# Kernel optimization log

Hardware: AMD Instinct MI355X
Metric: run time of the kernel (lower is better)

The kernel has to match this reference:

```python
import jax, jax.numpy as jnp
import numpy as np
from jax import lax

TS = 8          # texture cube resolution (hardcoded texture_size=8)
CHUNK = 336     # 13776 = 336 * 41, faces processed in scan chunks
EPS = 1e-8
INF = 1e30


def _project(vertices, K, R, t):
    # camera_mode='projection': v_cam = v @ R^T + t, then pinhole via K
    v_cam = vertices @ R.T + t            # [N,3]
    z = v_cam[:, 2]                        # [N]
    uvw = v_cam @ K.T                      # [N,3]
    xy = uvw[:, :2] / z[:, None]           # [N,2] pixel coords
    return xy, z


def _rasterize(xy, z, faces, H, W):
    # hard z-buffer rasterization, scanning over face chunks
    P = H * W
    px = jnp.arange(W, dtype=jnp.float32) + 0.5
    py = jnp.arange(H, dtype=jnp.float32) + 0.5
    pix_x = jnp.broadcast_to(px[None, :], (H, W)).reshape(P)
    pix_y = jnp.broadcast_to(py[:, None], (H, W)).reshape(P)

    nF = faces.shape[0]
    nchunks = nF // CHUNK
    fch = faces.reshape(nchunks, CHUNK, 3)
    offs = (jnp.arange(nchunks) * CHUNK).astype(jnp.int32)

    def step(carry, inp):
        zbuf, fid, wbuf = carry
        fc, off = inp
        tri = xy[fc]                       # [C,3,2]
        tz = z[fc]                         # [C,3]
        x0, y0 = tri[:, 0, 0][:, None], tri[:, 0, 1][:, None]
        x1, y1 = tri[:, 1, 0][:, None], tri[:, 1, 1][:, None]
        x2, y2 = tri[:, 2, 0][:, None], tri[:, 2, 1][:, None]
        denom = (y1 - y2) * (x0 - x2) + (x2 - x1) * (y0 - y2)   # [C,1]
        dsafe = jnp.where(jnp.abs(denom) > EPS, denom, 1.0)
        w0 = ((y1 - y2) * (pix_x - x2) + (x2 - x1) * (pix_y - y2)) / dsafe  # [C,P]
        w1 = ((y2 - y0) * (pix_x - x2) + (x0 - x2) * (pix_y - y2)) / dsafe
        w2 = 1.0 - w0 - w1
        valid = (jnp.abs(denom) > EPS) & (tz.min(axis=1, keepdims=True) > EPS)
        inside = (w0 >= 0) & (w1 >= 0) & (w2 >= 0) & valid
        # perspective-correct depth: 1/z = sum_i w_i / z_i
        inv_z = w0 / tz[:, 0:1] + w1 / tz[:, 1:2] + w2 / tz[:, 2:3]
        depth = jnp.where(inside & (inv_z > EPS), 1.0 / jnp.maximum(inv_z, EPS), INF)
        best = jnp.argmin(depth, axis=0)                         # [P]
        dmin = jnp.take_along_axis(depth, best[None, :], 0)[0]
        w0g = jnp.take_along_axis(w0, best[None, :], 0)[0]
        w1g = jnp.take_along_axis(w1, best[None, :], 0)[0]
        w2g = 1.0 - w0g - w1g
        wz = tz[best]                                            # [P,3]
        wc = jnp.stack([w0g, w1g, w2g], -1) / jnp.maximum(wz, EPS)
        wc = wc / jnp.maximum(wc.sum(-1, keepdims=True), EPS)    # persp-correct bary
        upd = dmin < zbuf
        zbuf = jnp.where(upd, dmin, zbuf)
        fid = jnp.where(upd, off + best.astype(jnp.int32), fid)
        wbuf = jnp.where(upd[:, None], wc, wbuf)
        return (zbuf, fid, wbuf), None

    init = (jnp.full((P,), INF, jnp.float32),
            jnp.full((P,), -1, jnp.int32),
            jnp.zeros((P, 3), jnp.float32))
    (zbuf, fid, wbuf), _ = lax.scan(step, init, (fch, offs))
    return fid, wbuf


def _sample_texture(texture, fid, bary):
    # trilinear sample of per-face texture cube [F,TS,TS,TS,3] at barycentric coords
    valid = fid >= 0
    f = jnp.where(valid, fid, 0)
    pos = jnp.clip(bary, 0.0, 1.0) * (TS - 1)
    i0 = jnp.clip(jnp.floor(pos), 0, TS - 2).astype(jnp.int32)   # [P,3]
    fr = pos - i0.astype(jnp.float32)
    flat = texture.reshape(-1, 3)
    base = f * (TS * TS * TS)
    out = jnp.zeros((fid.shape[0], 3), texture.dtype)
    for d0 in (0, 1):
        for d1 in (0, 1):
            for d2 in (0, 1):
                idx = base + (i0[:, 0] + d0) * TS * TS + (i0[:, 1] + d1) * TS + (i0[:, 2] + d2)
                w = ((fr[:, 0] if d0 else 1.0 - fr[:, 0])
                     * (fr[:, 1] if d1 else 1.0 - fr[:, 1])
                     * (fr[:, 2] if d2 else 1.0 - fr[:, 2]))
                out = out + w[:, None] * flat[idx]
    return out, valid


def setup_inputs() -> dict:
    key = jax.random.key(0)
    ks = jax.random.split(key, 4)
    n_verts, n_faces = 6890, 13776
    rs = 256
    vertices = 0.3 * jax.random.normal(ks[0], (n_verts, 3), jnp.float32)
    focal, c = 280.0, rs / 2.0
    K = jnp.array([[focal, 0.0, c], [0.0, focal, c], [0.0, 0.0, 1.0]], jnp.float32)
    R = jnp.eye(3, dtype=jnp.float32)
    t = jnp.array([0.0, 0.0, 2.5], jnp.float32)
    bgcolor = 255.0 * jax.random.uniform(ks[1], (3,), jnp.float32)
    texture = jax.random.normal(ks[2], (n_faces, TS, TS, TS, 3), jnp.float32)
    faces = jax.random.randint(ks[3], (n_faces, 3), 0, n_verts, jnp.int32)
    return {"vertices": vertices, "K": K, "R": R, "t": t, "bgcolor": bgcolor,
            "texture": texture, "faces": faces, "img_size": rs, "render_size": rs}


def reference(vertices, K, R, t, bgcolor, texture, faces, img_size, render_size):
    H = W = int(render_size)
    tex = jax.nn.relu(texture)             # F.relu(self.texture)
    bg = bgcolor / 255.0                   # bgcolor / 255
    xy, z = _project(vertices, K, R, t)
    fid, bary = _rasterize(xy, z, faces, H, W)
    rgb, valid = _sample_texture(tex, fid, bary)
    alpha = valid.astype(jnp.float32)
    rgb = jnp.where(valid[:, None], rgb, bg[None, :])
    rgb_patches = rgb.reshape(1, H, W, 3)      # rgbs.permute(0,2,3,1)
    alpha_patches = alpha.reshape(1, H, W)
    return rgb_patches, alpha_patches
```

## Files before the change

kernel.cpp:

```cpp
#include <hip/hip_runtime.h>
#include <math.h>

#define EPSF 1e-8f
#define BIGF 1e30f
#define NSEG 64

__device__ __forceinline__ float fastrcp(float x) {
    float y;
    asm("v_rcp_f32 %0, %1" : "=v"(y) : "v"(x));
    return y;
}

__device__ __forceinline__ void project_vert(
    const float* __restrict__ Km, const float* __restrict__ Rm,
    const float* __restrict__ tv,
    float vx, float vy, float vz, float& X, float& Y, float& Z)
{
    float a;
    a = __fadd_rn(__fmul_rn(vx, Rm[0]), __fmul_rn(vy, Rm[1]));
    a = __fadd_rn(a, __fmul_rn(vz, Rm[2]));
    float c0 = __fadd_rn(a, tv[0]);
    a = __fadd_rn(__fmul_rn(vx, Rm[3]), __fmul_rn(vy, Rm[4]));
    a = __fadd_rn(a, __fmul_rn(vz, Rm[5]));
    float c1 = __fadd_rn(a, tv[1]);
    a = __fadd_rn(__fmul_rn(vx, Rm[6]), __fmul_rn(vy, Rm[7]));
    a = __fadd_rn(a, __fmul_rn(vz, Rm[8]));
    float c2 = __fadd_rn(a, tv[2]);

    float u0 = __fadd_rn(__fadd_rn(__fmul_rn(c0, Km[0]), __fmul_rn(c1, Km[1])),
                         __fmul_rn(c2, Km[2]));
    float u1 = __fadd_rn(__fadd_rn(__fmul_rn(c0, Km[3]), __fmul_rn(c1, Km[4])),
                         __fmul_rn(c2, Km[5]));
    X = __fdiv_rn(u0, c2);
    Y = __fdiv_rn(u1, c2);
    Z = c2;
}

__global__ __launch_bounds__(64) void k_prep(
    const float* __restrict__ verts,
    const float* __restrict__ Km, const float* __restrict__ Rm,
    const float* __restrict__ tv, const int* __restrict__ faces,
    float4* __restrict__ rec, float4* __restrict__ box,
    unsigned long long* __restrict__ zwin, int nF, int P)
{
    int f = blockIdx.x * blockDim.x + threadIdx.x;
    int stride = gridDim.x * blockDim.x;
    unsigned long long initpk =
        ((unsigned long long)__float_as_uint(BIGF) << 32) | 0x7fffffffu;
    for (int i = f; i < P; i += stride) zwin[i] = initpk;
    if (f >= nF) return;

    int ia = faces[3*f+0], ib = faces[3*f+1], ic = faces[3*f+2];
    float x0, y0, z0, x1, y1, z1, x2, y2, z2;
    project_vert(Km, Rm, tv, verts[3*ia], verts[3*ia+1], verts[3*ia+2], x0, y0, z0);
    project_vert(Km, Rm, tv, verts[3*ib], verts[3*ib+1], verts[3*ib+2], x1, y1, z1);
    project_vert(Km, Rm, tv, verts[3*ic], verts[3*ic+1], verts[3*ic+2], x2, y2, z2);

    float y12 = __fsub_rn(y1, y2);
    float x21 = __fsub_rn(x2, x1);
    float y20 = __fsub_rn(y2, y0);
    float x02 = __fsub_rn(x0, x2);
    float y02 = __fsub_rn(y0, y2);
    float dn  = __fadd_rn(__fmul_rn(y12, x02), __fmul_rn(x21, y02));
    float zmin = fminf(fminf(z0, z1), z2);
    bool valid = (fabsf(dn) > EPSF) && (zmin > EPSF);
    float bxmin, bxmax, bymin, bymax;
    if (valid) {
        bxmin = fminf(fminf(x0, x1), x2) - 0.5f;
        bxmax = fmaxf(fmaxf(x0, x1), x2) + 0.5f;
        bymin = fminf(fminf(y0, y1), y2) - 0.5f;
        bymax = fmaxf(fmaxf(y0, y1), y2) + 0.5f;
    } else {
        bxmin = BIGF; bxmax = -BIGF; bymin = BIGF; bymax = -BIGF;
    }
    rec[3*f+0] = make_float4(y12, x21, y20, x02);
    rec[3*f+1] = make_float4(x2, y2, dn, z0);
    rec[3*f+2] = make_float4(z1, z2, __int_as_float(f), zmin);
    box[f]     = make_float4(bxmin, bxmax, bymin, bymax);
}

__global__ __launch_bounds__(256) void k_raster(
    const float4* __restrict__ rec, const float4* __restrict__ box,
    unsigned long long* __restrict__ zwin,
    int nF, int W, int H, int tilesX, int nTiles)
{
    __shared__ float  sM[4][64];
    __shared__ float4 sZ[4][64];
    __shared__ float4 sE[4][64][2];
    int wid  = threadIdx.x >> 6;
    int lane = threadIdx.x & 63;
    int tile = blockIdx.x * 4 + wid;
    if (tile >= nTiles) return;

    int segw = (nF + NSEG - 1) / NSEG;
    int fbeg = blockIdx.y * segw;
    int fend = min(nF, fbeg + segw);
    if (fbeg >= fend) return;

    int tileX = tile % tilesX, tileY = tile / tilesX;
    int tx = lane & 7, ty = lane >> 3;
    int pxi = tileX * 8 + tx;
    int pyi = tileY * 8 + ty;
    bool inimg = (pxi < W) && (pyi < H);
    float px = (float)pxi + 0.5f;
    float py = (float)pyi + 0.5f;
    float rx0 = (float)(tileX * 8) + 0.5f;
    float rx1 = rx0 + 7.0f;
    float ry0 = (float)(tileY * 8) + 0.5f;
    float ry1 = ry0 + 7.0f;
    float cx  = (float)(tileX * 8) + 4.0f;
    float cy  = (float)(tileY * 8) + 4.0f;

    int pidx = inimg ? (pyi * W + pxi) : 0;
    unsigned long long seed = zwin[pidx];
    float bd = __uint_as_float((unsigned)(seed >> 32));
    int   bf = (int)(unsigned)(seed & 0xffffffffu);

    const float4* sM4g = (const float4*)sM[wid];

    float4 nb = box[min(fbeg + lane, nF - 1)];

    for (int base = fbeg; base < fend; base += 64) {
        float4 cb = nb;
        if (base + 64 < fend) nb = box[min(base + 64 + lane, nF - 1)];
        int f = base + lane;
        bool pass = (f < fend) &&
                    (cb.x <= rx1) && (cb.y >= rx0) && (cb.z <= ry1) && (cb.w >= ry0);
        float4 r0, r1, r2;
        if (pass) {
            r0 = rec[3*f+0];
            r1 = rec[3*f+1];
            float s  = (r1.z > 0.0f) ? 1.0f : -1.0f;
            float dx = cx - r1.x, dy = cy - r1.y;
            float n0c = r0.x * dx + r0.y * dy;
            float n1c = r0.z * dx + r0.w * dy;
            float t0 = s * n0c + 3.6f * (fabsf(r0.x) + fabsf(r0.y));
            float t1 = s * n1c + 3.6f * (fabsf(r0.z) + fabsf(r0.w));
            float t2 = s * (r1.z - n0c - n1c)
                     + 3.6f * (fabsf(r0.x + r0.z) + fabsf(r0.y + r0.w));
            pass = (t0 >= 0.0f) && (t1 >= 0.0f) && (t2 >= 0.0f);
        }
        if (pass) r2 = rec[3*f+2];
        unsigned long long m = __ballot(pass);
        if (pass) {
            int slot = __popcll(m & ((1ull << lane) - 1ull));
            sM[wid][slot]    = r2.w;
            sZ[wid][slot]    = r2;
            sE[wid][slot][0] = r0;
            sE[wid][slot][1] = r1;
        }
        int scnt = (int)__popcll(m);

        for (int g = 0; g < scnt; g += 4) {
            float4 z4 = sM4g[g >> 2];
            float zg = fminf(fminf(z4.x, z4.y), fminf(z4.z, z4.w));
            if (!__any(zg <= __fmul_rn(bd, 1.001f))) continue;
            int jend = min(scnt, g + 4);
            for (int j = g; j < jend; ++j) {
                if (!__any(sM[wid][j] <= __fmul_rn(bd, 1.001f))) continue;
                float4 r2b = sZ[wid][j];
                float4 r0b = sE[wid][j][0];
                float4 r1b = sE[wid][j][1];

                float dx = __fsub_rn(px, r1b.x);
                float dy = __fsub_rn(py, r1b.y);
                float n0 = __fadd_rn(__fmul_rn(r0b.x, dx), __fmul_rn(r0b.y, dy));
                float n1 = __fadd_rn(__fmul_rn(r0b.z, dx), __fmul_rn(r0b.w, dy));
                float dn = r1b.z;
                bool dpos = dn > 0.0f;
                bool in0 = (n0 == 0.0f) || ((n0 > 0.0f) == dpos);
                bool in1 = (n1 == 0.0f) || ((n1 > 0.0f) == dpos);
                bool cand = in0 && in1;
                if (cand) {
                    float rdn = fastrcp(dn);
                    float w0a = n0 * rdn, w1a = n1 * rdn;
                    float w2a = 1.0f - w0a - w1a;
                    float ss  = 1.0f + fabsf(w0a) + fabsf(w1a);
                    cand = (w2a >= -1e-4f * ss);
                    if (cand) {
                        float iza = w0a * fastrcp(r1b.w) + w1a * fastrcp(r2b.x)
                                  + w2a * fastrcp(r2b.y);
                        float da  = fastrcp(iza);
                        cand = (da <= __fmul_rn(bd, 1.001f));
                    }
                }
                if (cand) {
                    float w0 = __fdiv_rn(n0, dn);
                    float w1 = __fdiv_rn(n1, dn);
                    float w2 = __fsub_rn(__fsub_rn(1.0f, w0), w1);
                    if (w2 >= 0.0f) {
                        float a  = __fdiv_rn(w0, r1b.w);
                        float b2 = __fdiv_rn(w1, r2b.x);
                        float c  = __fdiv_rn(w2, r2b.y);
                        float iz = __fadd_rn(__fadd_rn(a, b2), c);
                        if (iz > EPSF) {
                            float d = __fdiv_rn(1.0f, iz);
                            int  fc = __float_as_int(r2b.z);
                            if ((d < bd) || ((d == bd) && (fc < bf))) {
                                bd = d; bf = fc;
                            }
                        }
                    }
                }
            }
        }
    }

    unsigned long long pk =
        ((unsigned long long)__float_as_uint(bd) << 32) | (unsigned int)bf;
    if (inimg && pk < seed) atomicMin(&zwin[pidx], pk);
}

__global__ __launch_bounds__(128) void k_shade(
    const float4* __restrict__ rec,
    const unsigned long long* __restrict__ zwin,
    const float* __restrict__ tex, const float* __restrict__ bgc,
    float* __restrict__ out, int W, int H)
{
    int p = blockIdx.x * blockDim.x + threadIdx.x;
    int P = W * H;
    if (p >= P) return;
    int pxi = p % W, pyi = p / W;
    float px = (float)pxi + 0.5f;
    float py = (float)pyi + 0.5f;

    unsigned long long pk = zwin[p];
    float o0, o1, o2, oa;
    if ((unsigned)(pk >> 32) != __float_as_uint(BIGF)) {
        int f = (int)(pk & 0xffffffffu);
        float4 r0 = rec[3*f+0];
        float4 r1 = rec[3*f+1];
        float4 r2 = rec[3*f+2];
        float dx = __fsub_rn(px, r1.x);
        float dy = __fsub_rn(py, r1.y);
        float n0 = __fadd_rn(__fmul_rn(r0.x, dx), __fmul_rn(r0.y, dy));
        float n1 = __fadd_rn(__fmul_rn(r0.z, dx), __fmul_rn(r0.w, dy));
        float w0 = __fdiv_rn(n0, r1.z);
        float w1 = __fdiv_rn(n1, r1.z);
        float w2 = __fsub_rn(__fsub_rn(1.0f, w0), w1);
        float c0 = __fdiv_rn(w0, fmaxf(r1.w, EPSF));
        float c1 = __fdiv_rn(w1, fmaxf(r2.x, EPSF));
        float c2 = __fdiv_rn(w2, fmaxf(r2.y, EPSF));
        float s  = __fadd_rn(__fadd_rn(c0, c1), c2);
        s = fmaxf(s, EPSF);
        c0 = __fdiv_rn(c0, s);
        c1 = __fdiv_rn(c1, s);
        c2 = __fdiv_rn(c2, s);
        float p0 = __fmul_rn(fminf(fmaxf(c0, 0.0f), 1.0f), 7.0f);
        float p1 = __fmul_rn(fminf(fmaxf(c1, 0.0f), 1.0f), 7.0f);
        float p2 = __fmul_rn(fminf(fmaxf(c2, 0.0f), 1.0f), 7.0f);
        int i0 = (int)floorf(p0); i0 = i0 < 0 ? 0 : (i0 > 6 ? 6 : i0);
        int i1 = (int)floorf(p1); i1 = i1 < 0 ? 0 : (i1 > 6 ? 6 : i1);
        int i2 = (int)floorf(p2); i2 = i2 < 0 ? 0 : (i2 > 6 ? 6 : i2);
        float f0 = __fsub_rn(p0, (float)i0);
        float f1 = __fsub_rn(p1, (float)i1);
        float f2 = __fsub_rn(p2, (float)i2);
        const float* tb = tex + (size_t)f * (512 * 3);
        float a0 = 0.0f, a1 = 0.0f, a2 = 0.0f;
        #pragma unroll
        for (int d0 = 0; d0 < 2; ++d0) {
            float wx = d0 ? f0 : __fsub_rn(1.0f, f0);
            #pragma unroll
            for (int d1 = 0; d1 < 2; ++d1) {
                float wy = d1 ? f1 : __fsub_rn(1.0f, f1);
                #pragma unroll
                for (int d2 = 0; d2 < 2; ++d2) {
                    float wz = d2 ? f2 : __fsub_rn(1.0f, f2);
                    float w = __fmul_rn(__fmul_rn(wx, wy), wz);
                    int idx = (((i0 + d0) << 6) + ((i1 + d1) << 3) + (i2 + d2)) * 3;
                    a0 = __fadd_rn(a0, __fmul_rn(w, fmaxf(tb[idx + 0], 0.0f)));
                    a1 = __fadd_rn(a1, __fmul_rn(w, fmaxf(tb[idx + 1], 0.0f)));
                    a2 = __fadd_rn(a2, __fmul_rn(w, fmaxf(tb[idx + 2], 0.0f)));
                }
            }
        }
        o0 = a0; o1 = a1; o2 = a2; oa = 1.0f;
    } else {
        o0 = __fdiv_rn(bgc[0], 255.0f);
        o1 = __fdiv_rn(bgc[1], 255.0f);
        o2 = __fdiv_rn(bgc[2], 255.0f);
        oa = 0.0f;
    }
    out[3*p+0] = o0;
    out[3*p+1] = o1;
    out[3*p+2] = o2;
    out[(size_t)P*3 + p] = oa;
}

extern "C" void kernel_launch(void* const* d_in, const int* in_sizes, int n_in,
                              void* d_out, int out_size, void* d_ws, size_t ws_size,
                              hipStream_t stream)
{
    const float* verts = (const float*)d_in[0];
    const float* Km    = (const float*)d_in[1];
    const float* Rm    = (const float*)d_in[2];
    const float* tv    = (const float*)d_in[3];
    const float* bgc   = (const float*)d_in[4];
    const float* tex   = (const float*)d_in[5];
    const int*   faces = (const int*)d_in[6];
    int nF = in_sizes[6] / 3;
    int P = out_size / 4;
    int W = (int)(sqrt((double)P) + 0.5);
    int H = W;
    int tilesX = (W + 7) / 8, tilesY = (H + 7) / 8;
    int nTiles = tilesX * tilesY;

    char* ws = (char*)d_ws;
    size_t o = 0;
    auto al = [](size_t x) { return (x + 255) & ~(size_t)255; };
    float4* rec = (float4*)(ws + o); o = al(o + (size_t)nF * 48);
    float4* box = (float4*)(ws + o); o = al(o + (size_t)nF * 16);
    unsigned long long* zwin = (unsigned long long*)(ws + o);
    o = al(o + (size_t)P * 8);
    (void)ws_size; (void)n_in;

    k_prep<<<dim3((nF + 63) / 64), dim3(64), 0, stream>>>(
        verts, Km, Rm, tv, faces, rec, box, zwin, nF, P);
    dim3 g((nTiles + 3) / 4, NSEG, 1);
    k_raster<<<g, dim3(256), 0, stream>>>(
        rec, box, zwin, nF, W, H, tilesX, nTiles);
    k_shade<<<dim3((P + 127) / 128), dim3(128), 0, stream>>>(
        rec, zwin, tex, bgc, (float*)d_out, W, H);
}
```

Baseline: 86.59 us.

## Depth-sort faces into bins and cull raster segments by minimum depth

Faces are histogrammed by minimum depth, prefix-scanned, and scattered into depth order, so each raster segment covers a narrow depth range. Each segment's minimum depth is recorded, which lets a whole wave exit early once all its pixels already hold a closer hit. Per-face culling now uses a packed tile-range record plus a depth test instead of float bounding-box compares. This adds three small kernels, a memset, and atomics. Ordering within a bin is nondeterministic, so the choice among equal-depth faces could change when tie-breaking depends on face order.

After: 143.3 us. 65.5% more time.

```diff
diff --git a/kernel.cpp b/kernel.cpp
--- a/kernel.cpp
+++ b/kernel.cpp
@@ -4,6 +4,7 @@
 #define EPSF 1e-8f
 #define BIGF 1e30f
 #define NSEG 64
+#define NBIN 256
 
 __device__ __forceinline__ float fastrcp(float x) {
     float y;
@@ -36,51 +37,134 @@
     Z = c2;
 }
 
+__device__ __forceinline__ int zbin(bool valid, float zmin)
+{
+    if (!valid) return NBIN - 1;
+    int b = (int)((zmin - 1.0f) * 64.0f);
+    return b < 0 ? 0 : (b > NBIN - 1 ? NBIN - 1 : b);
+}
+
+__device__ __forceinline__ bool tile_range(float4 b, int tilesX, int tilesY,
+                                           int& tx0, int& tx1, int& ty0, int& ty1)
+{
+    if (b.x > b.y) return false;
+    float fx0 = fmaxf(0.0f, ceilf((b.x - 7.5f - 1e-3f) * 0.125f));
+    float fx1 = fminf((float)(tilesX - 1), floorf((b.y - 0.5f + 1e-3f) * 0.125f));
+    float fy0 = fmaxf(0.0f, ceilf((b.z - 7.5f - 1e-3f) * 0.125f));
+    float fy1 = fminf((float)(tilesY - 1), floorf((b.w - 0.5f + 1e-3f) * 0.125f));
+    if (fx0 > fx1 || fy0 > fy1) return false;
+    tx0 = (int)fx0; tx1 = (int)fx1; ty0 = (int)fy0; ty1 = (int)fy1;
+    return true;
+}
+
 __global__ __launch_bounds__(64) void k_prep(
     const float* __restrict__ verts,
     const float* __restrict__ Km, const float* __restrict__ Rm,
     const float* __restrict__ tv, const int* __restrict__ faces,
     float4* __restrict__ rec, float4* __restrict__ box,
-    unsigned long long* __restrict__ zwin, int nF, int P)
-{
+    unsigned long long* __restrict__ zwin, unsigned* __restrict__ segminz,
+    unsigned* __restrict__ hist, int nF, int P)
+{
+    __shared__ unsigned sh[NBIN];
+    for (int i = threadIdx.x; i < NBIN; i += 64) sh[i] = 0;
+    __syncthreads();
+
     int f = blockIdx.x * blockDim.x + threadIdx.x;
     int stride = gridDim.x * blockDim.x;
     unsigned long long initpk =
         ((unsigned long long)__float_as_uint(BIGF) << 32) | 0x7fffffffu;
     for (int i = f; i < P; i += stride) zwin[i] = initpk;
+    for (int i = f; i < NSEG; i += stride) segminz[i] = 0x7f7fffffu;
+
+    if (f < nF) {
+        int ia = faces[3*f+0], ib = faces[3*f+1], ic = faces[3*f+2];
+        float x0, y0, z0, x1, y1, z1, x2, y2, z2;
+        project_vert(Km, Rm, tv, verts[3*ia], verts[3*ia+1], verts[3*ia+2], x0, y0, z0);
+        project_vert(Km, Rm, tv, verts[3*ib], verts[3*ib+1], verts[3*ib+2], x1, y1, z1);
+        project_vert(Km, Rm, tv, verts[3*ic], verts[3*ic+1], verts[3*ic+2], x2, y2, z2);
+
+        float y12 = __fsub_rn(y1, y2);
+        float x21 = __fsub_rn(x2, x1);
+        float y20 = __fsub_rn(y2, y0);
+        float x02 = __fsub_rn(x0, x2);
+        float y02 = __fsub_rn(y0, y2);
+        float dn  = __fadd_rn(__fmul_rn(y12, x02), __fmul_rn(x21, y02));
+        float zmin = fminf(fminf(z0, z1), z2);
+        bool valid = (fabsf(dn) > EPSF) && (zmin > EPSF);
+        float bxmin, bxmax, bymin, bymax;
+        if (valid) {
+            bxmin = fminf(fminf(x0, x1), x2) - 0.5f;
+            bxmax = fmaxf(fmaxf(x0, x1), x2) + 0.5f;
+            bymin = fminf(fminf(y0, y1), y2) - 0.5f;
+            bymax = fmaxf(fmaxf(y0, y1), y2) + 0.5f;
+        } else {
+            bxmin = BIGF; bxmax = -BIGF; bymin = BIGF; bymax = -BIGF;
+        }
+        rec[3*f+0] = make_float4(y12, x21, y20, x02);
+        rec[3*f+1] = make_float4(x2, y2, dn, z0);
+        rec[3*f+2] = make_float4(z1, z2, __int_as_float(f), zmin);
+        box[f]     = make_float4(bxmin, bxmax, bymin, bymax);
+        atomicAdd(&sh[zbin(valid, zmin)], 1u);
+    }
+    __syncthreads();
+    for (int i = threadIdx.x; i < NBIN; i += 64) {
+        unsigned c = sh[i];
+        if (c) atomicAdd(&hist[i], c);
+    }
+}
+
+__global__ __launch_bounds__(NBIN) void k_scan(const unsigned* __restrict__ hist,
+                                               unsigned* __restrict__ off)
+{
+    __shared__ unsigned s[NBIN];
+    int t = threadIdx.x;
+    s[t] = hist[t];
+    __syncthreads();
+    for (int d = 1; d < NBIN; d <<= 1) {
+        unsigned a = (t >= d) ? s[t - d] : 0;
+        __syncthreads();
+        s[t] += a;
+        __syncthreads();
+    }
+    off[t + 1] = s[t];
+    if (t == 0) off[0] = 0;
+}
+
+__global__ __launch_bounds__(64) void k_scatter(
+    const float4* __restrict__ rec, const float4* __restrict__ box,
+    const unsigned* __restrict__ off, unsigned* __restrict__ cur,
+    float4* __restrict__ rec2, uint2* __restrict__ cullrec,
+    unsigned* __restrict__ segminz,
+    int nF, int tilesX, int tilesY, int segw)
+{
+    int f = blockIdx.x * blockDim.x + threadIdx.x;
     if (f >= nF) return;
-
-    int ia = faces[3*f+0], ib = faces[3*f+1], ic = faces[3*f+2];
-    float x0, y0, z0, x1, y1, z1, x2, y2, z2;
-    project_vert(Km, Rm, tv, verts[3*ia], verts[3*ia+1], verts[3*ia+2], x0, y0, z0);
-    project_vert(Km, Rm, tv, verts[3*ib], verts[3*ib+1], verts[3*ib+2], x1, y1, z1);
-    project_vert(Km, Rm, tv, verts[3*ic], verts[3*ic+1], verts[3*ic+2], x2, y2, z2);
-
-    float y12 = __fsub_rn(y1, y2);
-    float x21 = __fsub_rn(x2, x1);
-    float y20 = __fsub_rn(y2, y0);
-    float x02 = __fsub_rn(x0, x2);
-    float y02 = __fsub_rn(y0, y2);
-    float dn  = __fadd_rn(__fmul_rn(y12, x02), __fmul_rn(x21, y02));
-    float zmin = fminf(fminf(z0, z1), z2);
-    bool valid = (fabsf(dn) > EPSF) && (zmin > EPSF);
-    float bxmin, bxmax, bymin, bymax;
+    float4 b  = box[f];
+    float4 r2 = rec[3*f+2];
+    float zmin = r2.w;
+    bool valid = (b.x <= b.y);
+    int bin = zbin(valid, zmin);
+    unsigned slot = off[bin] + atomicAdd(&cur[bin], 1u);
+    rec2[3*slot+0] = rec[3*f+0];
+    rec2[3*slot+1] = rec[3*f+1];
+    rec2[3*slot+2] = r2;
+    unsigned tr = 0x00FF00FFu;
     if (valid) {
-        bxmin = fminf(fminf(x0, x1), x2) - 0.5f;
-        bxmax = fmaxf(fmaxf(x0, x1), x2) + 0.5f;
-        bymin = fminf(fminf(y0, y1), y2) - 0.5f;
-        bymax = fmaxf(fmaxf(y0, y1), y2) + 0.5f;
-    } else {
-        bxmin = BIGF; bxmax = -BIGF; bymin = BIGF; bymax = -BIGF;
-    }
-    rec[3*f+0] = make_float4(y12, x21, y20, x02);
-    rec[3*f+1] = make_float4(x2, y2, dn, z0);
-    rec[3*f+2] = make_float4(z1, z2, __int_as_float(f), zmin);
-    box[f]     = make_float4(bxmin, bxmax, bymin, bymax);
+        int tx0, tx1, ty0, ty1;
+        if (tile_range(b, tilesX, tilesY, tx0, tx1, ty0, ty1)) {
+            tx0 = min(tx0, 255); tx1 = min(tx1, 255);
+            ty0 = min(ty0, 255); ty1 = min(ty1, 255);
+            tr = (unsigned)tx0 | ((unsigned)tx1 << 8)
+               | ((unsigned)ty0 << 16) | ((unsigned)ty1 << 24);
+            atomicMin(&segminz[slot / segw], __float_as_uint(zmin));
+        }
+    }
+    cullrec[slot] = make_uint2(tr, __float_as_uint(zmin));
 }
 
 __global__ __launch_bounds__(256) void k_raster(
-    const float4* __restrict__ rec, const float4* __restrict__ box,
+    const float4* __restrict__ rec2, const uint2* __restrict__ cullrec,
+    const unsigned* __restrict__ segminz,
     unsigned long long* __restrict__ zwin,
     int nF, int W, int H, int tilesX, int nTiles)
 {
@@ -98,16 +182,13 @@
     if (fbeg >= fend) return;
 
     int tileX = tile % tilesX, tileY = tile / tilesX;
+    int tXc = min(tileX, 255), tYc = min(tileY, 255);
     int tx = lane & 7, ty = lane >> 3;
     int pxi = tileX * 8 + tx;
     int pyi = tileY * 8 + ty;
     bool inimg = (pxi < W) && (pyi < H);
     float px = (float)pxi + 0.5f;
     float py = (float)pyi + 0.5f;
-    float rx0 = (float)(tileX * 8) + 0.5f;
-    float rx1 = rx0 + 7.0f;
-    float ry0 = (float)(tileY * 8) + 0.5f;
-    float ry1 = ry0 + 7.0f;
     float cx  = (float)(tileX * 8) + 4.0f;
     float cy  = (float)(tileY * 8) + 4.0f;
 
@@ -116,20 +197,33 @@
     float bd = __uint_as_float((unsigned)(seed >> 32));
     int   bf = (int)(unsigned)(seed & 0xffffffffu);
 
+    float thr = __fmul_rn(bd, 1.001f);
+    #pragma unroll
+    for (int o = 32; o >= 1; o >>= 1) thr = fmaxf(thr, __shfl_xor(thr, o));
+    if (__uint_as_float(segminz[blockIdx.y]) > thr) return;
+
     const float4* sM4g = (const float4*)sM[wid];
 
-    float4 nb = box[min(fbeg + lane, nF - 1)];
+    uint2 nb = cullrec[min(fbeg + lane, nF - 1)];
 
     for (int base = fbeg; base < fend; base += 64) {
-        float4 cb = nb;
-        if (base + 64 < fend) nb = box[min(base + 64 + lane, nF - 1)];
+        uint2 cb = nb;
+        if (base + 64 < fend) nb = cullrec[min(base + 64 + lane, nF - 1)];
+        thr = __fmul_rn(bd, 1.001f);
+        #pragma unroll
+        for (int o = 32; o >= 1; o >>= 1) thr = fmaxf(thr, __shfl_xor(thr, o));
+
         int f = base + lane;
-        bool pass = (f < fend) &&
-                    (cb.x <= rx1) && (cb.y >= rx0) && (cb.z <= ry1) && (cb.w >= ry0);
+        unsigned tr = cb.x;
+        float zm = __uint_as_float(cb.y);
+        bool pass = (f < fend)
+                 && tXc >= (int)(tr & 255) && tXc <= (int)((tr >> 8) & 255)
+                 && tYc >= (int)((tr >> 16) & 255) && tYc <= (int)(tr >> 24)
+                 && (zm <= thr);
         float4 r0, r1, r2;
         if (pass) {
-            r0 = rec[3*f+0];
-            r1 = rec[3*f+1];
+            r0 = rec2[3*f+0];
+            r1 = rec2[3*f+1];
             float s  = (r1.z > 0.0f) ? 1.0f : -1.0f;
             float dx = cx - r1.x, dy = cy - r1.y;
             float n0c = r0.x * dx + r0.y * dy;
@@ -140,11 +234,11 @@
                      + 3.6f * (fabsf(r0.x + r0.z) + fabsf(r0.y + r0.w));
             pass = (t0 >= 0.0f) && (t1 >= 0.0f) && (t2 >= 0.0f);
         }
-        if (pass) r2 = rec[3*f+2];
+        if (pass) r2 = rec2[3*f+2];
         unsigned long long m = __ballot(pass);
         if (pass) {
             int slot = __popcll(m & ((1ull << lane) - 1ull));
-            sM[wid][slot]    = r2.w;
+            sM[wid][slot]    = zm;
             sZ[wid][slot]    = r2;
             sE[wid][slot][0] = r0;
             sE[wid][slot][1] = r1;
@@ -304,21 +398,35 @@
     int H = W;
     int tilesX = (W + 7) / 8, tilesY = (H + 7) / 8;
     int nTiles = tilesX * tilesY;
+    int segw = (nF + NSEG - 1) / NSEG;
 
     char* ws = (char*)d_ws;
     size_t o = 0;
     auto al = [](size_t x) { return (x + 255) & ~(size_t)255; };
-    float4* rec = (float4*)(ws + o); o = al(o + (size_t)nF * 48);
-    float4* box = (float4*)(ws + o); o = al(o + (size_t)nF * 16);
+    float4* rec  = (float4*)(ws + o); o = al(o + (size_t)nF * 48);
+    float4* box  = (float4*)(ws + o); o = al(o + (size_t)nF * 16);
+    float4* rec2 = (float4*)(ws + o); o = al(o + (size_t)nF * 48);
+    uint2*  cullrec = (uint2*)(ws + o); o = al(o + (size_t)nF * 8);
     unsigned long long* zwin = (unsigned long long*)(ws + o);
     o = al(o + (size_t)P * 8);
+    unsigned* hist = (unsigned*)(ws + o);
+    unsigned* cur  = hist + NBIN;
+    o = al(o + (size_t)NBIN * 8);
+    unsigned* offb = (unsigned*)(ws + o);
+    o = al(o + (size_t)(NBIN + 1) * 4);
+    unsigned* segminz = (unsigned*)(ws + o);
+    o = al(o + (size_t)NSEG * 4);
     (void)ws_size; (void)n_in;
 
+    hipMemsetAsync(hist, 0, (size_t)NBIN * 8, stream);
     k_prep<<<dim3((nF + 63) / 64), dim3(64), 0, stream>>>(
-        verts, Km, Rm, tv, faces, rec, box, zwin, nF, P);
+        verts, Km, Rm, tv, faces, rec, box, zwin, segminz, hist, nF, P);
+    k_scan<<<dim3(1), dim3(NBIN), 0, stream>>>(hist, offb);
+    k_scatter<<<dim3((nF + 63) / 64), dim3(64), 0, stream>>>(
+        rec, box, offb, cur, rec2, cullrec, segminz, nF, tilesX, tilesY, segw);
     dim3 g((nTiles + 3) / 4, NSEG, 1);
     k_raster<<<g, dim3(256), 0, stream>>>(
-        rec, box, zwin, nF, W, H, tilesX, nTiles);
+        rec2, cullrec, segminz, zwin, nF, W, H, tilesX, nTiles);
     k_shade<<<dim3((P + 127) / 128), dim3(128), 0, stream>>>(
         rec, zwin, tex, bgc, (float*)d_out, W, H);
 }
```
